# Performance work log

Measured on AMD Instinct MI355X. Metric: run time of the kernel, lower is better.

## Reference

```python
import jax, jax.numpy as jnp
import numpy as np

OUT, IN = 4096, 4096  # W_shape
K, BLOCK = 256, 8     # codebook entries, block dim


def setup_inputs() -> dict:
    key = jax.random.key(0)
    k1, k2, k3, k4, k5 = jax.random.split(key, 5)
    x = jax.random.normal(k1, (4, 2048, IN), dtype=jnp.float32)
    centroids = jax.random.normal(k2, (K, BLOCK), dtype=jnp.float32)
    labels = jax.random.randint(k3, (OUT * IN // BLOCK,), 0, K, dtype=jnp.int64)
    scale = jax.random.uniform(k4, (IN,), dtype=jnp.float32)
    bias = jax.random.normal(k5, (OUT,), dtype=jnp.float32)
    return {"x": x, "centroids": centroids, "labels": labels, "scale": scale, "bias": bias}


def reference(x, centroids, labels, scale, bias):
    # VQ weight decompression: gather codebook vectors, reshape to [OUT, IN]
    W_smooth = centroids[labels].reshape(OUT, IN)
    # F.linear(x * scale, W, bias) == (x*scale) @ W.T + bias
    return jnp.einsum('bsi,oi->bso', x * scale, W_smooth) + bias
```

## Files before the change

kernel.cpp:

```cpp
#include <hip/hip_runtime.h>
#include <stdint.h>

#define M_DIM 8192
#define N_DIM 4096
#define K_DIM 4096
#define NUM_VQ (N_DIM * K_DIM / 8)
#define NUM_X  (M_DIM * K_DIM)
#define VQ_BLOCKS (NUM_VQ / 256)
#define CVT_BLOCKS (NUM_X / 8 / 256)

#define BK     64
#define DEPTH  2
#define TILES  (K_DIM / BK)
#define ROUNDS (TILES / DEPTH)

#define AS1 __attribute__((address_space(1)))
#define AS3 __attribute__((address_space(3)))

typedef __attribute__((ext_vector_type(4))) float f32x4;
typedef __attribute__((ext_vector_type(8))) short bf16x8;
typedef unsigned short u16;

__device__ inline unsigned short f2bf(float f) {
    union { float f; unsigned int i; } v; v.f = f;
    unsigned int x = v.i;
    return (unsigned short)((x + 0x7FFFu + ((x >> 16) & 1u)) >> 16);
}

__global__ void prep_w(const int* __restrict__ labels,
                       const float* __restrict__ centroids,
                       const float* __restrict__ scale,
                       u16* __restrict__ Ws) {
    int lane = threadIdx.x & 63;
    int probe = labels[2 * lane + 1];
    bool is64 = (__ballot(probe != 0) == 0ull);
    int i = blockIdx.x * 256 + threadIdx.x;
    int lab = is64 ? labels[2 * i] : labels[i];
    int kb = i & 511;
    f32x4 c0 = ((const f32x4*)centroids)[2 * lab];
    f32x4 c1 = ((const f32x4*)centroids)[2 * lab + 1];
    f32x4 s0 = ((const f32x4*)scale)[2 * kb];
    f32x4 s1 = ((const f32x4*)scale)[2 * kb + 1];
    bf16x8 o;
#pragma unroll
    for (int j = 0; j < 4; ++j) {
        o[j]     = (short)f2bf(c0[j] * s0[j]);
        o[4 + j] = (short)f2bf(c1[j] * s1[j]);
    }
    ((bf16x8*)Ws)[i] = o;
}

__global__ void prep_x(const float* __restrict__ x, u16* __restrict__ Xb) {
    int i = blockIdx.x * 256 + threadIdx.x;
    f32x4 a = ((const f32x4*)x)[2 * i];
    f32x4 c = ((const f32x4*)x)[2 * i + 1];
    bf16x8 o;
#pragma unroll
    for (int j = 0; j < 4; ++j) { o[j] = (short)f2bf(a[j]); o[4 + j] = (short)f2bf(c[j]); }
    ((bf16x8*)Xb)[i] = o;
}

__global__ __launch_bounds__(384, 3)
void gemm_bias(const u16* __restrict__ A, const u16* __restrict__ B,
               const float* __restrict__ bias, float* __restrict__ C) {
    __shared__ u16 buf[DEPTH * 16384];
    __shared__ int ready[DEPTH];
    __shared__ int done[DEPTH];

    const int tid  = threadIdx.x;
    const int wave = tid >> 6;
    const int lane = tid & 63;
    const int bm = blockIdx.y * 128;
    const int bn = blockIdx.x * 128;

    if (tid < DEPTH) done[tid] = 0;
    else if (tid < 2 * DEPTH) ready[tid - DEPTH] = 0;
    __syncthreads();

    if (wave >= 4) {
        const int s = wave - 4;
        u16* stA = buf + s * 16384;
        u16* stB = stA + 8192;
        const int prow = lane >> 3;
        const int scol = ((lane & 7) ^ prow) * 8;
        const u16* baseA = A + (size_t)(bm + prow) * K_DIM + scol;
        const u16* baseB = B + (size_t)(bn + prow) * K_DIM + scol;

        for (int r = 0; r < ROUNDS; ++r) {
            const int kt = r * DEPTH + s;
            while (__hip_atomic_load(&done[s], __ATOMIC_ACQUIRE,
                                     __HIP_MEMORY_SCOPE_WORKGROUP) < 4 * r)
                __builtin_amdgcn_s_sleep(1);
            const u16* gA = baseA + kt * BK;
            const u16* gB = baseB + kt * BK;
#pragma unroll
            for (int j = 0; j < 16; ++j)
                __builtin_amdgcn_global_load_lds(
                    (const AS1 void*)(gA + (size_t)(8 * j) * K_DIM),
                    (AS3 void*)(stA + j * 512), 16, 0, 0);
#pragma unroll
            for (int j = 0; j < 16; ++j)
                __builtin_amdgcn_global_load_lds(
                    (const AS1 void*)(gB + (size_t)(8 * j) * K_DIM),
                    (AS3 void*)(stB + j * 512), 16, 0, 0);
            asm volatile("s_waitcnt vmcnt(0)" ::: "memory");
            __hip_atomic_store(&ready[s], r + 1, __ATOMIC_RELEASE,
                               __HIP_MEMORY_SCOPE_WORKGROUP);
        }
        return;
    }

    const int wm = (wave >> 1) * 64;
    const int wn = (wave & 1) * 64;
    const int fm = lane & 15;
    const int pc0 = (((lane >> 4)    ) ^ (lane & 7)) * 8;
    const int pc1 = (((lane >> 4) | 4) ^ (lane & 7)) * 8;

    f32x4 acc[4][4];
#pragma unroll
    for (int i = 0; i < 4; ++i)
#pragma unroll
        for (int j = 0; j < 4; ++j)
            acc[i][j] = (f32x4){0.f, 0.f, 0.f, 0.f};

    for (int kt = 0; kt < TILES; ++kt) {
        const int s = kt & (DEPTH - 1);
        const int r = kt >> 1;
        while (__hip_atomic_load(&ready[s], __ATOMIC_ACQUIRE,
                                 __HIP_MEMORY_SCOPE_WORKGROUP) < r + 1)
            __builtin_amdgcn_s_sleep(1);
        const u16* stA = buf + s * 16384;
        const u16* stB = stA + 8192;

        bf16x8 a0[4], b0[4], a1[4], b1[4];
#pragma unroll
        for (int i = 0; i < 4; ++i) {
            a0[i] = *(const bf16x8*)&stA[(wm + i * 16 + fm) * 64 + pc0];
            a1[i] = *(const bf16x8*)&stA[(wm + i * 16 + fm) * 64 + pc1];
        }
#pragma unroll
        for (int j = 0; j < 4; ++j) {
            b0[j] = *(const bf16x8*)&stB[(wn + j * 16 + fm) * 64 + pc0];
            b1[j] = *(const bf16x8*)&stB[(wn + j * 16 + fm) * 64 + pc1];
        }

        if (lane == 0)
            __hip_atomic_fetch_add(&done[s], 1, __ATOMIC_RELEASE,
                                   __HIP_MEMORY_SCOPE_WORKGROUP);

#pragma unroll
        for (int i = 0; i < 4; ++i)
#pragma unroll
            for (int j = 0; j < 4; ++j) {
                acc[i][j] = __builtin_amdgcn_mfma_f32_16x16x32_bf16(
                    a0[i], b0[j], acc[i][j], 0, 0, 0);
                acc[i][j] = __builtin_amdgcn_mfma_f32_16x16x32_bf16(
                    a1[i], b1[j], acc[i][j], 0, 0, 0);
            }
    }

    float biasv[4];
#pragma unroll
    for (int j = 0; j < 4; ++j)
        biasv[j] = bias[bn + wn + j * 16 + (lane & 15)];

    const int crow0 = bm + wm + (lane >> 4) * 4;
    const int ccol0 = bn + wn + (lane & 15);
#pragma unroll
    for (int i = 0; i < 4; ++i)
#pragma unroll
        for (int r = 0; r < 4; ++r) {
            size_t rowoff = (size_t)(crow0 + i * 16 + r) * N_DIM;
#pragma unroll
            for (int j = 0; j < 4; ++j)
                C[rowoff + ccol0 + j * 16] = acc[i][j][r] + biasv[j];
        }
}

extern "C" void kernel_launch(void* const* d_in, const int* in_sizes, int n_in,
                              void* d_out, int out_size, void* d_ws, size_t ws_size,
                              hipStream_t stream) {
    const float* x         = (const float*)d_in[0];
    const float* centroids = (const float*)d_in[1];
    const int*   labels    = (const int*)d_in[2];
    const float* scale     = (const float*)d_in[3];
    const float* bias      = (const float*)d_in[4];
    float* out             = (float*)d_out;

    u16* Ws = (u16*)d_ws;
    u16* Xb = (u16*)((char*)d_ws + (size_t)NUM_VQ * 16);

    prep_w<<<VQ_BLOCKS, 256, 0, stream>>>(labels, centroids, scale, Ws);
    prep_x<<<CVT_BLOCKS, 256, 0, stream>>>(x, Xb);

    dim3 grid(N_DIM / 128, M_DIM / 128);
    gemm_bias<<<grid, 384, 0, stream>>>(Xb, Ws, bias, out);
}
```

Before: 520.9 us.

## Split LDS fragment loads into two halves to cut registers and raise occupancy

The consumer waves now load only the first k-half of the A/B fragments, run its 16 MFMAs, then load the second half and run the rest. This halves the live fragment registers so launch bounds can target 4 blocks per CU instead of 3. MFMA sections are wrapped in s_setprio and fenced with a sched_barrier. The producer's done signal now comes after both halves are read, which delays buffer release and exposes LDS latency within each wave in exchange for higher occupancy. LDS use per block (64KB) may still cap residency, so the extra occupancy may not materialize.

```diff
diff --git a/kernel.cpp b/kernel.cpp
--- a/kernel.cpp
+++ b/kernel.cpp
@@ -60,7 +60,7 @@
     ((bf16x8*)Xb)[i] = o;
 }
 
-__global__ __launch_bounds__(384, 3)
+__global__ __launch_bounds__(384, 4)
 void gemm_bias(const u16* __restrict__ A, const u16* __restrict__ B,
                const float* __restrict__ bias, float* __restrict__ C) {
     __shared__ u16 buf[DEPTH * 16384];
@@ -132,31 +132,44 @@
         const u16* stA = buf + s * 16384;
         const u16* stB = stA + 8192;
 
-        bf16x8 a0[4], b0[4], a1[4], b1[4];
-#pragma unroll
-        for (int i = 0; i < 4; ++i) {
-            a0[i] = *(const bf16x8*)&stA[(wm + i * 16 + fm) * 64 + pc0];
-            a1[i] = *(const bf16x8*)&stA[(wm + i * 16 + fm) * 64 + pc1];
-        }
-#pragma unroll
-        for (int j = 0; j < 4; ++j) {
-            b0[j] = *(const bf16x8*)&stB[(wn + j * 16 + fm) * 64 + pc0];
-            b1[j] = *(const bf16x8*)&stB[(wn + j * 16 + fm) * 64 + pc1];
-        }
+        bf16x8 af[4], bfr[4];
+#pragma unroll
+        for (int i = 0; i < 4; ++i)
+            af[i] = *(const bf16x8*)&stA[(wm + i * 16 + fm) * 64 + pc0];
+#pragma unroll
+        for (int j = 0; j < 4; ++j)
+            bfr[j] = *(const bf16x8*)&stB[(wn + j * 16 + fm) * 64 + pc0];
+
+        __builtin_amdgcn_s_setprio(1);
+#pragma unroll
+        for (int i = 0; i < 4; ++i)
+#pragma unroll
+            for (int j = 0; j < 4; ++j)
+                acc[i][j] = __builtin_amdgcn_mfma_f32_16x16x32_bf16(
+                    af[i], bfr[j], acc[i][j], 0, 0, 0);
+        __builtin_amdgcn_s_setprio(0);
+
+        __builtin_amdgcn_sched_barrier(0);
+
+#pragma unroll
+        for (int i = 0; i < 4; ++i)
+            af[i] = *(const bf16x8*)&stA[(wm + i * 16 + fm) * 64 + pc1];
+#pragma unroll
+        for (int j = 0; j < 4; ++j)
+            bfr[j] = *(const bf16x8*)&stB[(wn + j * 16 + fm) * 64 + pc1];
 
         if (lane == 0)
             __hip_atomic_fetch_add(&done[s], 1, __ATOMIC_RELEASE,
                                    __HIP_MEMORY_SCOPE_WORKGROUP);
 
-#pragma unroll
-        for (int i = 0; i < 4; ++i)
-#pragma unroll
-            for (int j = 0; j < 4; ++j) {
+        __builtin_amdgcn_s_setprio(1);
+#pragma unroll
+        for (int i = 0; i < 4; ++i)
+#pragma unroll
+            for (int j = 0; j < 4; ++j)
                 acc[i][j] = __builtin_amdgcn_mfma_f32_16x16x32_bf16(
-                    a0[i], b0[j], acc[i][j], 0, 0, 0);
-                acc[i][j] = __builtin_amdgcn_mfma_f32_16x16x32_bf16(
-                    a1[i], b1[j], acc[i][j], 0, 0, 0);
-            }
+                    af[i], bfr[j], acc[i][j], 0, 0, 0);
+        __builtin_amdgcn_s_setprio(0);
     }
 
     float biasv[4];
```

New measurement: 542.7 us. 4.2% more time.

## Rewrite GEMM with 256x256 tiles, barrier-phased pipeline and XCD-aware block mapping

Applied to the files above, without the earlier changes.

Replaces the producer/consumer warp-specialized 128x128 GEMM with a 256x256 tile kernel of 8 waves. Every wave both issues global-to-LDS loads and runs MFMAs, in an explicitly scheduled 8-phase double-buffered pipeline synchronised with s_barrier and vmcnt waits. It also remaps block IDs across XCDs for locality and raises MFMA priority with s_setprio. The larger tile cuts global/LDS traffic per FLOP, at the cost of higher register pressure, a full 128KB LDS footprint and a rigid schedule.

```diff
diff --git a/kernel.cpp b/kernel.cpp
--- a/kernel.cpp
+++ b/kernel.cpp
@@ -9,10 +9,9 @@
 #define VQ_BLOCKS (NUM_VQ / 256)
 #define CVT_BLOCKS (NUM_X / 8 / 256)
 
-#define BK     64
-#define DEPTH  2
-#define TILES  (K_DIM / BK)
-#define ROUNDS (TILES / DEPTH)
+#define BM 256
+#define BN 256
+#define BK 64
 
 #define AS1 __attribute__((address_space(1)))
 #define AS3 __attribute__((address_space(3)))
@@ -60,120 +59,134 @@
     ((bf16x8*)Xb)[i] = o;
 }
 
-__global__ __launch_bounds__(384, 3)
+template <int Q>
+__device__ __forceinline__ void mfma16(f32x4 (&acc)[8][4], const bf16x8 (&a)[2][2],
+                                       const bf16x8 (&b)[4][2]) {
+    __builtin_amdgcn_s_setprio(1);
+#pragma unroll
+    for (int mm = 0; mm < 2; ++mm)
+#pragma unroll
+        for (int n = 0; n < 4; ++n)
+#pragma unroll
+            for (int ks = 0; ks < 2; ++ks)
+                acc[Q * 2 + mm][n] = __builtin_amdgcn_mfma_f32_16x16x32_bf16(
+                    a[mm][ks], b[n][ks], acc[Q * 2 + mm][n], 0, 0, 0);
+    __builtin_amdgcn_s_setprio(0);
+}
+
+__global__ __launch_bounds__(512, 2)
 void gemm_bias(const u16* __restrict__ A, const u16* __restrict__ B,
                const float* __restrict__ bias, float* __restrict__ C) {
-    __shared__ u16 buf[DEPTH * 16384];
-    __shared__ int ready[DEPTH];
-    __shared__ int done[DEPTH];
-
-    const int tid  = threadIdx.x;
-    const int wave = tid >> 6;
-    const int lane = tid & 63;
-    const int bm = blockIdx.y * 128;
-    const int bn = blockIdx.x * 128;
-
-    if (tid < DEPTH) done[tid] = 0;
-    else if (tid < 2 * DEPTH) ready[tid - DEPTH] = 0;
-    __syncthreads();
-
-    if (wave >= 4) {
-        const int s = wave - 4;
-        u16* stA = buf + s * 16384;
-        u16* stB = stA + 8192;
-        const int prow = lane >> 3;
-        const int scol = ((lane & 7) ^ prow) * 8;
-        const u16* baseA = A + (size_t)(bm + prow) * K_DIM + scol;
-        const u16* baseB = B + (size_t)(bn + prow) * K_DIM + scol;
-
-        for (int r = 0; r < ROUNDS; ++r) {
-            const int kt = r * DEPTH + s;
-            while (__hip_atomic_load(&done[s], __ATOMIC_ACQUIRE,
-                                     __HIP_MEMORY_SCOPE_WORKGROUP) < 4 * r)
-                __builtin_amdgcn_s_sleep(1);
-            const u16* gA = baseA + kt * BK;
-            const u16* gB = baseB + kt * BK;
-#pragma unroll
-            for (int j = 0; j < 16; ++j)
-                __builtin_amdgcn_global_load_lds(
-                    (const AS1 void*)(gA + (size_t)(8 * j) * K_DIM),
-                    (AS3 void*)(stA + j * 512), 16, 0, 0);
-#pragma unroll
-            for (int j = 0; j < 16; ++j)
-                __builtin_amdgcn_global_load_lds(
-                    (const AS1 void*)(gB + (size_t)(8 * j) * K_DIM),
-                    (AS3 void*)(stB + j * 512), 16, 0, 0);
-            asm volatile("s_waitcnt vmcnt(0)" ::: "memory");
-            __hip_atomic_store(&ready[s], r + 1, __ATOMIC_RELEASE,
-                               __HIP_MEMORY_SCOPE_WORKGROUP);
-        }
-        return;
+    __shared__ u16 buf[65536];
+
+    const int tid = threadIdx.x;
+    const int w   = tid >> 6;
+    const int l   = tid & 63;
+
+    const int bid = blockIdx.x;
+    const int wg  = (bid & 7) * 64 + (bid >> 3);
+    const int bm  = (wg >> 4) * BM;
+    const int bn  = (wg & 15) * BN;
+
+    const int srow = w * 16 + (l >> 3);
+    const int scol = ((l & 7) ^ ((l >> 3) & 7)) * 8;
+    const u16* Ag = A + (size_t)(bm + srow) * K_DIM + scol;
+    const u16* Bg = B + (size_t)(bn + srow) * K_DIM + scol;
+
+#define STAGE(c, mat, hh, t) do {                                              \
+    const u16* _g = ((mat) ? Bg : Ag) + (size_t)(hh) * 128 * K_DIM +           \
+                    (size_t)(t) * BK;                                          \
+    u16* _l = buf + (c) * 32768 + (mat) * 16384 + (hh) * 8192 + w * 1024;      \
+    __builtin_amdgcn_global_load_lds((const AS1 void*)_g, (AS3 void*)_l,       \
+                                     16, 0, 0);                                \
+    __builtin_amdgcn_global_load_lds((const AS1 void*)(_g + (size_t)8 * K_DIM),\
+                                     (AS3 void*)(_l + 512), 16, 0, 0);         \
+} while (0)
+
+    const int wm  = (w >> 2) * 128;
+    const int wn  = (w & 3) * 64;
+    const int fm  = l & 15;
+    const int fm7 = fm & 7;
+    const int hi  = l >> 4;
+
+#define LDA_(c, m, ks) (*(const bf16x8*)&buf[(c) * 32768 +                      \
+    (wm + (m) * 16 + fm) * 64 + (((hi + 4 * (ks)) ^ fm7) * 8)])
+#define LDB_(c, n, ks) (*(const bf16x8*)&buf[(c) * 32768 + 16384 +              \
+    (wn + (n) * 16 + fm) * 64 + (((hi + 4 * (ks)) ^ fm7) * 8)])
+
+#define READS(c, q) do {                                                        \
+    if ((q) == 0) {                                                             \
+        b[0][0] = LDB_(c, 0, 0); b[0][1] = LDB_(c, 0, 1);                       \
+        b[1][0] = LDB_(c, 1, 0); b[1][1] = LDB_(c, 1, 1);                       \
+        b[2][0] = LDB_(c, 2, 0); b[2][1] = LDB_(c, 2, 1);                       \
+        b[3][0] = LDB_(c, 3, 0); b[3][1] = LDB_(c, 3, 1);                       \
+    }                                                                           \
+    a[0][0] = LDA_(c, (q) * 2, 0);     a[0][1] = LDA_(c, (q) * 2, 1);           \
+    a[1][0] = LDA_(c, (q) * 2 + 1, 0); a[1][1] = LDA_(c, (q) * 2 + 1, 1);       \
+} while (0)
+
+#define PH(c, q, ...) do {                                                      \
+    READS(c, q);                                                                \
+    __VA_ARGS__                                                                 \
+    __builtin_amdgcn_s_barrier();                                               \
+    asm volatile("s_waitcnt lgkmcnt(0)" ::: "memory");                          \
+    __builtin_amdgcn_sched_barrier(0);                                          \
+    mfma16<q>(acc, a, b);                                                       \
+} while (0)
+#define ENDPH       __builtin_amdgcn_s_barrier()
+#define ENDPH_VM(N) do {                                                        \
+    asm volatile("s_waitcnt vmcnt(" #N ")" ::: "memory");                       \
+    __builtin_amdgcn_s_barrier();                                               \
+} while (0)
+
+    bf16x8 a[2][2], b[4][2];
+    f32x4 acc[8][4];
+#pragma unroll
+    for (int m = 0; m < 8; ++m)
+#pragma unroll
+        for (int n = 0; n < 4; ++n)
+            acc[m][n] = (f32x4){0.f, 0.f, 0.f, 0.f};
+
+    STAGE(0, 1, 0, 0); STAGE(0, 1, 1, 0);
+    STAGE(0, 0, 0, 0); STAGE(0, 0, 1, 0);
+    STAGE(1, 1, 0, 1); STAGE(1, 1, 1, 1);
+    asm volatile("s_waitcnt vmcnt(4)" ::: "memory");
+    __builtin_amdgcn_s_barrier();
+
+    for (int i = 0; i < 31; ++i) {
+        const int t1 = 2 * i + 1, t2 = 2 * i + 2, t3 = 2 * i + 3;
+        PH(0, 0, STAGE(1, 0, 0, t1););                     ENDPH;
+        PH(0, 1, STAGE(1, 0, 1, t1); STAGE(0, 1, 0, t2);); ENDPH;
+        PH(0, 2, STAGE(0, 1, 1, t2););                     ENDPH;
+        PH(0, 3, );                                        ENDPH_VM(4);
+        PH(1, 0, STAGE(0, 0, 0, t2););                     ENDPH;
+        PH(1, 1, STAGE(0, 0, 1, t2););                     ENDPH;
+        PH(1, 2, STAGE(1, 1, 0, t3););                     ENDPH;
+        PH(1, 3, STAGE(1, 1, 1, t3););                     ENDPH_VM(4);
     }
 
-    const int wm = (wave >> 1) * 64;
-    const int wn = (wave & 1) * 64;
-    const int fm = lane & 15;
-    const int pc0 = (((lane >> 4)    ) ^ (lane & 7)) * 8;
-    const int pc1 = (((lane >> 4) | 4) ^ (lane & 7)) * 8;
-
-    f32x4 acc[4][4];
-#pragma unroll
-    for (int i = 0; i < 4; ++i)
-#pragma unroll
-        for (int j = 0; j < 4; ++j)
-            acc[i][j] = (f32x4){0.f, 0.f, 0.f, 0.f};
-
-    for (int kt = 0; kt < TILES; ++kt) {
-        const int s = kt & (DEPTH - 1);
-        const int r = kt >> 1;
-        while (__hip_atomic_load(&ready[s], __ATOMIC_ACQUIRE,
-                                 __HIP_MEMORY_SCOPE_WORKGROUP) < r + 1)
-            __builtin_amdgcn_s_sleep(1);
-        const u16* stA = buf + s * 16384;
-        const u16* stB = stA + 8192;
-
-        bf16x8 a0[4], b0[4], a1[4], b1[4];
-#pragma unroll
-        for (int i = 0; i < 4; ++i) {
-            a0[i] = *(const bf16x8*)&stA[(wm + i * 16 + fm) * 64 + pc0];
-            a1[i] = *(const bf16x8*)&stA[(wm + i * 16 + fm) * 64 + pc1];
-        }
-#pragma unroll
-        for (int j = 0; j < 4; ++j) {
-            b0[j] = *(const bf16x8*)&stB[(wn + j * 16 + fm) * 64 + pc0];
-            b1[j] = *(const bf16x8*)&stB[(wn + j * 16 + fm) * 64 + pc1];
-        }
-
-        if (lane == 0)
-            __hip_atomic_fetch_add(&done[s], 1, __ATOMIC_RELEASE,
-                                   __HIP_MEMORY_SCOPE_WORKGROUP);
-
-#pragma unroll
-        for (int i = 0; i < 4; ++i)
-#pragma unroll
-            for (int j = 0; j < 4; ++j) {
-                acc[i][j] = __builtin_amdgcn_mfma_f32_16x16x32_bf16(
-                    a0[i], b0[j], acc[i][j], 0, 0, 0);
-                acc[i][j] = __builtin_amdgcn_mfma_f32_16x16x32_bf16(
-                    a1[i], b1[j], acc[i][j], 0, 0, 0);
-            }
-    }
+    PH(0, 0, STAGE(1, 0, 0, 63););  ENDPH;
+    PH(0, 1, STAGE(1, 0, 1, 63););  ENDPH;
+    PH(0, 2, );                     ENDPH;
+    PH(0, 3, );                     ENDPH_VM(0);
+    PH(1, 0, );                     ENDPH;
+    PH(1, 1, );                     ENDPH;
+    PH(1, 2, );                     ENDPH;
+    PH(1, 3, );
 
     float biasv[4];
 #pragma unroll
-    for (int j = 0; j < 4; ++j)
-        biasv[j] = bias[bn + wn + j * 16 + (lane & 15)];
-
-    const int crow0 = bm + wm + (lane >> 4) * 4;
-    const int ccol0 = bn + wn + (lane & 15);
-#pragma unroll
-    for (int i = 0; i < 4; ++i)
+    for (int n = 0; n < 4; ++n)
+        biasv[n] = bias[bn + wn + n * 16 + fm];
+    const int ccol0 = bn + wn + fm;
+#pragma unroll
+    for (int m = 0; m < 8; ++m)
 #pragma unroll
         for (int r = 0; r < 4; ++r) {
-            size_t rowoff = (size_t)(crow0 + i * 16 + r) * N_DIM;
-#pragma unroll
-            for (int j = 0; j < 4; ++j)
-                C[rowoff + ccol0 + j * 16] = acc[i][j][r] + biasv[j];
+            const size_t rowoff = (size_t)(bm + wm + m * 16 + hi * 4 + r) * N_DIM;
+#pragma unroll
+            for (int n = 0; n < 4; ++n)
+                C[rowoff + ccol0 + n * 16] = acc[m][n][r] + biasv[n];
         }
 }
 
@@ -193,6 +206,6 @@
     prep_w<<<VQ_BLOCKS, 256, 0, stream>>>(labels, centroids, scale, Ws);
     prep_x<<<CVT_BLOCKS, 256, 0, stream>>>(x, Xb);
 
-    dim3 grid(N_DIM / 128, M_DIM / 128);
-    gemm_bias<<<grid, 384, 0, stream>>>(Xb, Ws, bias, out);
-}
+    dim3 grid((M_DIM / BM) * (N_DIM / BN));
+    gemm_bias<<<grid, 512, 0, stream>>>(Xb, Ws, bias, out);
+}
```

Measured after the change: 464.4 us. 10.8% less time.
